# Kernel tuning notes

Measured on AMD Instinct MI355X. Metric: run time of the kernel, lower is better.

Reference implementation:

```python
import jax, jax.numpy as jnp
import numpy as np

SIG_T_TRAIN = 0.07
SIG_T_INFER = 0.07
EPS = 1e-12  # torch F.normalize eps


def _l2_normalize(x):
    # matches torch.nn.functional.normalize(x, dim=-1): x / max(||x||_2, eps)
    nrm = jnp.sqrt(jnp.sum(x * x, axis=-1, keepdims=True))
    return x / jnp.maximum(nrm, EPS)


def setup_inputs() -> dict:
    key = jax.random.key(0)
    k1, k2 = jax.random.split(key)
    v_feat = jax.random.normal(k1, (32, 16, 256, 512), dtype=jnp.float32)  # (b,n,t,d)
    t_feat = jax.random.normal(k2, (512, 512), dtype=jnp.float32)          # (c,d)
    return {"v_feat": v_feat, "t_feat": t_feat, "split": 1}


def reference(v_feat, t_feat, split):
    # split: 1 -> 'test' (normalize + sig_T_infer), 0 -> train (sig_T_train)
    if split == 1:
        tau = SIG_T_INFER
        v_feat = _l2_normalize(v_feat)
        t_feat = _l2_normalize(t_feat)
    else:
        tau = SIG_T_TRAIN
    # Original: dist = einsum('bntd,bmcd->bctnm', v, t_repeated)/tau, then mean over m, then n.
    # t_repeated is identical along m (a pure repeat), so mean over m is a no-op, and the
    # mean over n commutes with the linear contraction: reduce over n first, never
    # materializing the (b,c,t,n,m) tensor.
    v_mean = jnp.mean(v_feat, axis=1)  # (b,t,d)
    dist = jnp.einsum('btd,cd->bct', v_mean, t_feat) / tau  # (b,c,t)
    return dist
```

## Files before the change

kernel.cpp:

```cpp
#include <hip/hip_runtime.h>
#include <hip/hip_bf16.h>

typedef unsigned short u16;
typedef unsigned int u32;

typedef __bf16 bf16x8 __attribute__((ext_vector_type(8)));
typedef float f32x4 __attribute__((ext_vector_type(4)));

__device__ __forceinline__ u16 f2bf(float f) {
    u32 u = __float_as_uint(f);
    return (u16)((u + 0x7fffu + ((u >> 16) & 1u)) >> 16);
}

__global__ void vmean_kernel(const float* __restrict__ v,
                             const float* __restrict__ t_feat,
                             u16* __restrict__ vm,
                             u16* __restrict__ tn,
                             const int* __restrict__ splitp) {
    const int bx   = blockIdx.x;
    const int by   = blockIdx.y;
    const int tid  = threadIdx.x;
    const int w    = tid >> 6;
    const int lane = tid & 63;
    const int split = *splitp;

    if (by == 32) {
        if (w >= 2) return;
        const int row = bx * 2 + w;
        const float* rp = t_feat + (size_t)row * 512 + lane * 8;
        float4 x0 = *reinterpret_cast<const float4*>(rp);
        float4 x1 = *reinterpret_cast<const float4*>(rp + 4);
        float s = x0.x*x0.x + x0.y*x0.y + x0.z*x0.z + x0.w*x0.w
                + x1.x*x1.x + x1.y*x1.y + x1.z*x1.z + x1.w*x1.w;
#pragma unroll
        for (int off = 32; off > 0; off >>= 1) s += __shfl_xor(s, off, 64);
        float inv = 1.0f;
        if (split == 1) inv = 1.0f / fmaxf(sqrtf(s), 1e-12f);
        u32 p0 = (u32)f2bf(x0.x*inv) | ((u32)f2bf(x0.y*inv) << 16);
        u32 p1 = (u32)f2bf(x0.z*inv) | ((u32)f2bf(x0.w*inv) << 16);
        u32 p2 = (u32)f2bf(x1.x*inv) | ((u32)f2bf(x1.y*inv) << 16);
        u32 p3 = (u32)f2bf(x1.z*inv) | ((u32)f2bf(x1.w*inv) << 16);
        uint4 pk; pk.x = p0; pk.y = p1; pk.z = p2; pk.w = p3;
        reinterpret_cast<uint4*>(tn)[row * 64 + lane] = pk;
        return;
    }

    const int t = bx;
    const int b = by;
    __shared__ float lds[4 * 512];

    float acc[8];
#pragma unroll
    for (int i = 0; i < 8; i++) acc[i] = 0.f;

#pragma unroll
    for (int nn = 0; nn < 4; nn++) {
        const int n = w + nn * 4;
        const float* row = v + ((((size_t)b * 16 + n) * 256 + t) * 512) + lane * 8;
        float4 x0 = *reinterpret_cast<const float4*>(row);
        float4 x1 = *reinterpret_cast<const float4*>(row + 4);
        float s = x0.x*x0.x + x0.y*x0.y + x0.z*x0.z + x0.w*x0.w
                + x1.x*x1.x + x1.y*x1.y + x1.z*x1.z + x1.w*x1.w;
#pragma unroll
        for (int off = 32; off > 0; off >>= 1) s += __shfl_xor(s, off, 64);
        float inv = 1.0f;
        if (split == 1) inv = 1.0f / fmaxf(sqrtf(s), 1e-12f);
        acc[0] += x0.x * inv; acc[1] += x0.y * inv;
        acc[2] += x0.z * inv; acc[3] += x0.w * inv;
        acc[4] += x1.x * inv; acc[5] += x1.y * inv;
        acc[6] += x1.z * inv; acc[7] += x1.w * inv;
    }
#pragma unroll
    for (int i = 0; i < 8; i += 2) {
        float2 p; p.x = acc[i]; p.y = acc[i + 1];
        *reinterpret_cast<float2*>(&lds[w * 512 + lane * 8 + i]) = p;
    }
    __syncthreads();
    float2 r; r.x = 0.f; r.y = 0.f;
#pragma unroll
    for (int w2 = 0; w2 < 4; w2++) {
        float2 p = *reinterpret_cast<const float2*>(&lds[w2 * 512 + tid * 2]);
        r.x += p.x; r.y += p.y;
    }
    r.x *= (1.0f / 16.0f); r.y *= (1.0f / 16.0f);
    u32 packed = (u32)f2bf(r.x) | ((u32)f2bf(r.y) << 16);
    reinterpret_cast<u32*>(vm)[(((size_t)b * 256 + t) << 8) + tid] = packed;
}

__global__ __launch_bounds__(256) void gemm_kernel(const u16* __restrict__ tn,
                                                   const u16* __restrict__ vm,
                                                   float* __restrict__ out) {
    const int bx   = blockIdx.x;
    const int by   = blockIdx.y;
    const int b    = blockIdx.z;
    const int tid  = threadIdx.x;
    const int lane = tid & 63;
    const int wid  = tid >> 6;
    const int wm   = wid & 1;
    const int wn   = wid >> 1;
    const int quad = lane >> 4;
    const int l15  = lane & 15;

    __shared__ u16 At[128 * 72];
    __shared__ u16 Bt[64 * 72];

    const int c0 = bx * 128, t0 = by * 64;
    f32x4 acc[4][2] = {};

    const int lrow = tid >> 3;
    const int lcol = (tid & 7) * 8;

    const uint4* gA = reinterpret_cast<const uint4*>(tn);
    const uint4* gB = reinterpret_cast<const uint4*>(vm) + (size_t)b * 256 * 64;

    for (int k0 = 0; k0 < 512; k0 += 64) {
#pragma unroll
        for (int it = 0; it < 4; it++) {
            int row = lrow + it * 32;
            uint4 av = gA[(c0 + row) * 64 + (k0 >> 3) + (tid & 7)];
            *reinterpret_cast<uint4*>(&At[row * 72 + lcol]) = av;
        }
#pragma unroll
        for (int it = 0; it < 2; it++) {
            int row = lrow + it * 32;
            uint4 bv = gB[(t0 + row) * 64 + (k0 >> 3) + (tid & 7)];
            *reinterpret_cast<uint4*>(&Bt[row * 72 + lcol]) = bv;
        }
        __syncthreads();
#pragma unroll
        for (int kk = 0; kk < 64; kk += 32) {
            bf16x8 af[4], bfr[2];
#pragma unroll
            for (int i = 0; i < 4; i++)
                af[i] = *reinterpret_cast<const bf16x8*>(
                    &At[(wm * 64 + i * 16 + l15) * 72 + kk + quad * 8]);
#pragma unroll
            for (int j = 0; j < 2; j++)
                bfr[j] = *reinterpret_cast<const bf16x8*>(
                    &Bt[(wn * 32 + j * 16 + l15) * 72 + kk + quad * 8]);
#pragma unroll
            for (int i = 0; i < 4; i++)
#pragma unroll
                for (int j = 0; j < 2; j++)
                    acc[i][j] = __builtin_amdgcn_mfma_f32_16x16x32_bf16(
                        af[i], bfr[j], acc[i][j], 0, 0, 0);
        }
        __syncthreads();
    }

    const float s = 1.0f / 0.07f;
    float* ob = out + (size_t)b * 131072;
#pragma unroll
    for (int i = 0; i < 4; i++)
#pragma unroll
        for (int j = 0; j < 2; j++)
#pragma unroll
            for (int r = 0; r < 4; r++) {
                int c = c0 + wm * 64 + i * 16 + quad * 4 + r;
                int t = t0 + wn * 32 + j * 16 + l15;
                ob[c * 256 + t] = acc[i][j][r] * s;
            }
}

extern "C" void kernel_launch(void* const* d_in, const int* in_sizes, int n_in,
                              void* d_out, int out_size, void* d_ws, size_t ws_size,
                              hipStream_t stream) {
    const float* v_feat = (const float*)d_in[0];
    const float* t_feat = (const float*)d_in[1];
    const int*   splitp = (const int*)d_in[2];
    float* out = (float*)d_out;

    u16* tn = (u16*)d_ws;
    u16* vm = tn + 512 * 512;

    vmean_kernel<<<dim3(256, 33), dim3(256), 0, stream>>>(v_feat, t_feat, vm, tn, splitp);
    gemm_kernel<<<dim3(4, 4, 32), dim3(256), 0, stream>>>(tn, vm, out);
}
```

Before: 367.6 us.

## Fuse view-mean normalization and text GEMM into a single kernel

```diff
diff --git a/kernel.cpp b/kernel.cpp
--- a/kernel.cpp
+++ b/kernel.cpp
@@ -1,5 +1,4 @@
 #include <hip/hip_runtime.h>
-#include <hip/hip_bf16.h>
 
 typedef unsigned short u16;
 typedef unsigned int u32;
@@ -12,154 +11,103 @@
     return (u16)((u + 0x7fffu + ((u >> 16) & 1u)) >> 16);
 }
 
-__global__ void vmean_kernel(const float* __restrict__ v,
-                             const float* __restrict__ t_feat,
-                             u16* __restrict__ vm,
-                             u16* __restrict__ tn,
-                             const int* __restrict__ splitp) {
-    const int bx   = blockIdx.x;
-    const int by   = blockIdx.y;
+__device__ __forceinline__ float rowreduce64(float s) {
+#pragma unroll
+    for (int off = 32; off > 0; off >>= 1) s += __shfl_xor(s, off, 64);
+    return s;
+}
+
+constexpr int LDK = 520;
+
+__global__ __launch_bounds__(512, 2) void fused_kernel(
+    const float* __restrict__ v,
+    const float* __restrict__ tf,
+    float* __restrict__ out,
+    const int* __restrict__ splitp)
+{
+    const int b    = blockIdx.y;
+    const int t0   = blockIdx.x * 32;
     const int tid  = threadIdx.x;
     const int w    = tid >> 6;
     const int lane = tid & 63;
+    const int quad = lane >> 4;
+    const int l15  = lane & 15;
     const int split = *splitp;
 
-    if (by == 32) {
-        if (w >= 2) return;
-        const int row = bx * 2 + w;
-        const float* rp = t_feat + (size_t)row * 512 + lane * 8;
-        float4 x0 = *reinterpret_cast<const float4*>(rp);
-        float4 x1 = *reinterpret_cast<const float4*>(rp + 4);
-        float s = x0.x*x0.x + x0.y*x0.y + x0.z*x0.z + x0.w*x0.w
-                + x1.x*x1.x + x1.y*x1.y + x1.z*x1.z + x1.w*x1.w;
+    __shared__ u16 At[64 * LDK];
+    __shared__ u16 Bt[32 * LDK];
+
+    for (int tt = 0; tt < 4; tt++) {
+        const int tl = w * 4 + tt;
+        float acc[8];
 #pragma unroll
-        for (int off = 32; off > 0; off >>= 1) s += __shfl_xor(s, off, 64);
-        float inv = 1.0f;
-        if (split == 1) inv = 1.0f / fmaxf(sqrtf(s), 1e-12f);
-        u32 p0 = (u32)f2bf(x0.x*inv) | ((u32)f2bf(x0.y*inv) << 16);
-        u32 p1 = (u32)f2bf(x0.z*inv) | ((u32)f2bf(x0.w*inv) << 16);
-        u32 p2 = (u32)f2bf(x1.x*inv) | ((u32)f2bf(x1.y*inv) << 16);
-        u32 p3 = (u32)f2bf(x1.z*inv) | ((u32)f2bf(x1.w*inv) << 16);
-        uint4 pk; pk.x = p0; pk.y = p1; pk.z = p2; pk.w = p3;
-        reinterpret_cast<uint4*>(tn)[row * 64 + lane] = pk;
-        return;
+        for (int i = 0; i < 8; i++) acc[i] = 0.f;
+#pragma unroll 4
+        for (int n = 0; n < 16; n++) {
+            const float* row = v + (((size_t)(b * 16 + n) * 256 + (t0 + tl)) * 512) + lane * 8;
+            float4 x0 = *reinterpret_cast<const float4*>(row);
+            float4 x1 = *reinterpret_cast<const float4*>(row + 4);
+            float s = x0.x*x0.x + x0.y*x0.y + x0.z*x0.z + x0.w*x0.w
+                    + x1.x*x1.x + x1.y*x1.y + x1.z*x1.z + x1.w*x1.w;
+            s = rowreduce64(s);
+            float inv = 1.0f;
+            if (split == 1) inv = 1.0f / fmaxf(sqrtf(s), 1e-12f);
+            acc[0] += x0.x*inv; acc[1] += x0.y*inv;
+            acc[2] += x0.z*inv; acc[3] += x0.w*inv;
+            acc[4] += x1.x*inv; acc[5] += x1.y*inv;
+            acc[6] += x1.z*inv; acc[7] += x1.w*inv;
+        }
+        uint4 pk;
+        pk.x = (u32)f2bf(acc[0]*0.0625f) | ((u32)f2bf(acc[1]*0.0625f) << 16);
+        pk.y = (u32)f2bf(acc[2]*0.0625f) | ((u32)f2bf(acc[3]*0.0625f) << 16);
+        pk.z = (u32)f2bf(acc[4]*0.0625f) | ((u32)f2bf(acc[5]*0.0625f) << 16);
+        pk.w = (u32)f2bf(acc[6]*0.0625f) | ((u32)f2bf(acc[7]*0.0625f) << 16);
+        *reinterpret_cast<uint4*>(&Bt[tl * LDK + lane * 8]) = pk;
     }
 
-    const int t = bx;
-    const int b = by;
-    __shared__ float lds[4 * 512];
+    const int wm = w & 3;
+    const int wn = w >> 2;
+    const float sc = 1.0f / 0.07f;
+    float* ob = out + (size_t)b * 131072;
 
-    float acc[8];
+    for (int cc = 0; cc < 8; cc++) {
 #pragma unroll
-    for (int i = 0; i < 8; i++) acc[i] = 0.f;
+        for (int rr = 0; rr < 8; rr++) {
+            const int r = w * 8 + rr;
+            const float* rp = tf + (size_t)(cc * 64 + r) * 512 + lane * 8;
+            float4 x0 = *reinterpret_cast<const float4*>(rp);
+            float4 x1 = *reinterpret_cast<const float4*>(rp + 4);
+            float s = x0.x*x0.x + x0.y*x0.y + x0.z*x0.z + x0.w*x0.w
+                    + x1.x*x1.x + x1.y*x1.y + x1.z*x1.z + x1.w*x1.w;
+            s = rowreduce64(s);
+            float inv = 1.0f;
+            if (split == 1) inv = 1.0f / fmaxf(sqrtf(s), 1e-12f);
+            uint4 pk;
+            pk.x = (u32)f2bf(x0.x*inv) | ((u32)f2bf(x0.y*inv) << 16);
+            pk.y = (u32)f2bf(x0.z*inv) | ((u32)f2bf(x0.w*inv) << 16);
+            pk.z = (u32)f2bf(x1.x*inv) | ((u32)f2bf(x1.y*inv) << 16);
+            pk.w = (u32)f2bf(x1.z*inv) | ((u32)f2bf(x1.w*inv) << 16);
+            *reinterpret_cast<uint4*>(&At[r * LDK + lane * 8]) = pk;
+        }
+        __syncthreads();
+
+        f32x4 acc = {0.f, 0.f, 0.f, 0.f};
+#pragma unroll
+        for (int kk = 0; kk < 512; kk += 32) {
+            bf16x8 af = *reinterpret_cast<const bf16x8*>(
+                &At[(wm * 16 + l15) * LDK + kk + quad * 8]);
+            bf16x8 bf = *reinterpret_cast<const bf16x8*>(
+                &Bt[(wn * 16 + l15) * LDK + kk + quad * 8]);
+            acc = __builtin_amdgcn_mfma_f32_16x16x32_bf16(af, bf, acc, 0, 0, 0);
+        }
+        __syncthreads();
 
 #pragma unroll
-    for (int nn = 0; nn < 4; nn++) {
-        const int n = w + nn * 4;
-        const float* row = v + ((((size_t)b * 16 + n) * 256 + t) * 512) + lane * 8;
-        float4 x0 = *reinterpret_cast<const float4*>(row);
-        float4 x1 = *reinterpret_cast<const float4*>(row + 4);
-        float s = x0.x*x0.x + x0.y*x0.y + x0.z*x0.z + x0.w*x0.w
-                + x1.x*x1.x + x1.y*x1.y + x1.z*x1.z + x1.w*x1.w;
-#pragma unroll
-        for (int off = 32; off > 0; off >>= 1) s += __shfl_xor(s, off, 64);
-        float inv = 1.0f;
-        if (split == 1) inv = 1.0f / fmaxf(sqrtf(s), 1e-12f);
-        acc[0] += x0.x * inv; acc[1] += x0.y * inv;
-        acc[2] += x0.z * inv; acc[3] += x0.w * inv;
-        acc[4] += x1.x * inv; acc[5] += x1.y * inv;
-        acc[6] += x1.z * inv; acc[7] += x1.w * inv;
+        for (int r = 0; r < 4; r++) {
+            const int c = cc * 64 + wm * 16 + quad * 4 + r;
+            ob[c * 256 + (t0 + wn * 16 + l15)] = acc[r] * sc;
+        }
     }
-#pragma unroll
-    for (int i = 0; i < 8; i += 2) {
-        float2 p; p.x = acc[i]; p.y = acc[i + 1];
-        *reinterpret_cast<float2*>(&lds[w * 512 + lane * 8 + i]) = p;
-    }
-    __syncthreads();
-    float2 r; r.x = 0.f; r.y = 0.f;
-#pragma unroll
-    for (int w2 = 0; w2 < 4; w2++) {
-        float2 p = *reinterpret_cast<const float2*>(&lds[w2 * 512 + tid * 2]);
-        r.x += p.x; r.y += p.y;
-    }
-    r.x *= (1.0f / 16.0f); r.y *= (1.0f / 16.0f);
-    u32 packed = (u32)f2bf(r.x) | ((u32)f2bf(r.y) << 16);
-    reinterpret_cast<u32*>(vm)[(((size_t)b * 256 + t) << 8) + tid] = packed;
-}
-
-__global__ __launch_bounds__(256) void gemm_kernel(const u16* __restrict__ tn,
-                                                   const u16* __restrict__ vm,
-                                                   float* __restrict__ out) {
-    const int bx   = blockIdx.x;
-    const int by   = blockIdx.y;
-    const int b    = blockIdx.z;
-    const int tid  = threadIdx.x;
-    const int lane = tid & 63;
-    const int wid  = tid >> 6;
-    const int wm   = wid & 1;
-    const int wn   = wid >> 1;
-    const int quad = lane >> 4;
-    const int l15  = lane & 15;
-
-    __shared__ u16 At[128 * 72];
-    __shared__ u16 Bt[64 * 72];
-
-    const int c0 = bx * 128, t0 = by * 64;
-    f32x4 acc[4][2] = {};
-
-    const int lrow = tid >> 3;
-    const int lcol = (tid & 7) * 8;
-
-    const uint4* gA = reinterpret_cast<const uint4*>(tn);
-    const uint4* gB = reinterpret_cast<const uint4*>(vm) + (size_t)b * 256 * 64;
-
-    for (int k0 = 0; k0 < 512; k0 += 64) {
-#pragma unroll
-        for (int it = 0; it < 4; it++) {
-            int row = lrow + it * 32;
-            uint4 av = gA[(c0 + row) * 64 + (k0 >> 3) + (tid & 7)];
-            *reinterpret_cast<uint4*>(&At[row * 72 + lcol]) = av;
-        }
-#pragma unroll
-        for (int it = 0; it < 2; it++) {
-            int row = lrow + it * 32;
-            uint4 bv = gB[(t0 + row) * 64 + (k0 >> 3) + (tid & 7)];
-            *reinterpret_cast<uint4*>(&Bt[row * 72 + lcol]) = bv;
-        }
-        __syncthreads();
-#pragma unroll
-        for (int kk = 0; kk < 64; kk += 32) {
-            bf16x8 af[4], bfr[2];
-#pragma unroll
-            for (int i = 0; i < 4; i++)
-                af[i] = *reinterpret_cast<const bf16x8*>(
-                    &At[(wm * 64 + i * 16 + l15) * 72 + kk + quad * 8]);
-#pragma unroll
-            for (int j = 0; j < 2; j++)
-                bfr[j] = *reinterpret_cast<const bf16x8*>(
-                    &Bt[(wn * 32 + j * 16 + l15) * 72 + kk + quad * 8]);
-#pragma unroll
-            for (int i = 0; i < 4; i++)
-#pragma unroll
-                for (int j = 0; j < 2; j++)
-                    acc[i][j] = __builtin_amdgcn_mfma_f32_16x16x32_bf16(
-                        af[i], bfr[j], acc[i][j], 0, 0, 0);
-        }
-        __syncthreads();
-    }
-
-    const float s = 1.0f / 0.07f;
-    float* ob = out + (size_t)b * 131072;
-#pragma unroll
-    for (int i = 0; i < 4; i++)
-#pragma unroll
-        for (int j = 0; j < 2; j++)
-#pragma unroll
-            for (int r = 0; r < 4; r++) {
-                int c = c0 + wm * 64 + i * 16 + quad * 4 + r;
-                int t = t0 + wn * 32 + j * 16 + l15;
-                ob[c * 256 + t] = acc[i][j][r] * s;
-            }
 }
 
 extern "C" void kernel_launch(void* const* d_in, const int* in_sizes, int n_in,
@@ -170,9 +118,7 @@
     const int*   splitp = (const int*)d_in[2];
     float* out = (float*)d_out;
 
-    u16* tn = (u16*)d_ws;
-    u16* vm = tn + 512 * 512;
+    (void)d_ws; (void)ws_size;
 
-    vmean_kernel<<<dim3(256, 33), dim3(256), 0, stream>>>(v_feat, t_feat, vm, tn, splitp);
-    gemm_kernel<<<dim3(4, 4, 32), dim3(256), 0, stream>>>(tn, vm, out);
+    fused_kernel<<<dim3(8, 32), dim3(512), 0, stream>>>(v_feat, t_feat, out, splitp);
 }
```

Result: slower. 426.6 us (+16.0%).
